# Optimization experiments

Hardware: AMD Instinct MI355X
Metric: run time of the kernel (lower is better)

Reference implementation:

```python
import jax, jax.numpy as jnp
import numpy as np

EPS = 1e-5

def _ternary(w):
    # BitNet 1.58-bit: per-output-channel scale = median(|W|) (scale_op='median'),
    # quantize to {-1,0,1}*scale with straight-through estimator.
    s = jnp.maximum(jnp.median(jnp.abs(w), axis=(1, 2, 3), keepdims=True), EPS)
    q = jnp.clip(jnp.round(w / s), -1.0, 1.0) * s
    return w + jax.lax.stop_gradient(q - w)

def _conv3x3(x, w):
    # NCHW, OIHW, stride 1, pad 1 (spatial-preserving)
    return jax.lax.conv_general_dilated(
        x, _ternary(w), (1, 1), ((1, 1), (1, 1)),
        dimension_numbers=('NCHW', 'OIHW', 'NCHW'))

def _bn(y, g, b, m, v):
    # eval-mode BatchNorm2d folded to a single scale/shift
    inv = g / jnp.sqrt(v + EPS)
    return y * inv[None, :, None, None] + (b - m * inv)[None, :, None, None]

def _ssh(x, p):
    (w3, g3, b3, m3, v3,
     ws, gs, bs, ms, vs,
     w5, g5, b5, m5, v5,
     w7a, g7a, b7a, m7a, v7a,
     w7b, g7b, b7b, m7b, v7b) = p
    c3 = _bn(_conv3x3(x, w3), g3, b3, m3, v3)                      # [B, half, H, W]
    stem = jax.nn.silu(_bn(_conv3x3(x, ws), gs, bs, ms, vs))       # [B, quart, H, W]
    c5 = _bn(_conv3x3(stem, w5), g5, b5, m5, v5)                   # [B, quart, H, W]
    t = jax.nn.silu(_bn(_conv3x3(stem, w7a), g7a, b7a, m7a, v7a))
    c7 = _bn(_conv3x3(t, w7b), g7b, b7b, m7b, v7b)                 # [B, quart, H, W]
    return jax.nn.silu(jnp.concatenate((c3, c5, c7), axis=1))      # [B, out_ch, H, W]

def setup_inputs() -> dict:
    key = jax.random.key(0)
    B, CIN, H, W = 32, 256, 64, 64
    HALF, Q = 128, 64  # out_ch=256 -> half=128, quart=64
    d = {"x": jax.random.normal(jax.random.fold_in(key, 0), (B, CIN, H, W), jnp.float32)}

    def mk(i, o, c):
        k0, k1, k2, k3, k4 = jax.random.split(jax.random.fold_in(key, i), 5)
        return (jax.random.normal(k0, (o, c, 3, 3), jnp.float32) * 0.05,
                1.0 + 0.1 * jax.random.normal(k1, (o,), jnp.float32),   # gamma
                0.1 * jax.random.normal(k2, (o,), jnp.float32),          # beta
                0.1 * jax.random.normal(k3, (o,), jnp.float32),          # running mean
                0.5 + jax.random.uniform(k4, (o,), jnp.float32))         # running var > 0

    for name, (o, c), i in [("3", (HALF, CIN), 1), ("s", (Q, CIN), 2),
                            ("5", (Q, Q), 3), ("7a", (Q, Q), 4), ("7b", (Q, Q), 5)]:
        w, g, b, m, v = mk(i, o, c)
        d["w" + name] = w; d["g" + name] = g; d["b" + name] = b
        d["m" + name] = m; d["v" + name] = v
    return d

def reference(x,
              w3, g3, b3, m3, v3,
              ws, gs, bs, ms, vs,
              w5, g5, b5, m5, v5,
              w7a, g7a, b7a, m7a, v7a,
              w7b, g7b, b7b, m7b, v7b):
    return _ssh(x, (w3, g3, b3, m3, v3, ws, gs, bs, ms, vs,
                    w5, g5, b5, m5, v5, w7a, g7a, b7a, m7a, v7a,
                    w7b, g7b, b7b, m7b, v7b))
```

## Files before the change

kernel.cpp:

```cpp
#include <hip/hip_runtime.h>
#include <stdint.h>

#define EPSF 1e-5f

typedef __bf16 bf16;
typedef __attribute__((ext_vector_type(8))) __bf16 bf16x8;
typedef __attribute__((ext_vector_type(4))) float f32x4;

#define GL16(src, dst) __builtin_amdgcn_global_load_lds( \
    (const __attribute__((address_space(1))) void*)(src), \
    (__attribute__((address_space(3))) void*)(dst), 16, 0, 0)
#define MEMFENCE() asm volatile("" ::: "memory")

template<int N> __device__ __forceinline__ void vwait() {
  static_assert(N == 2 || N == 3 || N == 4 || N == 6, "unsupported vmcnt");
  if constexpr (N == 2) asm volatile("s_waitcnt vmcnt(2)" ::: "memory");
  else if constexpr (N == 3) asm volatile("s_waitcnt vmcnt(3)" ::: "memory");
  else if constexpr (N == 4) asm volatile("s_waitcnt vmcnt(4)" ::: "memory");
  else asm volatile("s_waitcnt vmcnt(6)" ::: "memory");
}

struct QArgs {
  const float* w[5];
  const float* g[5];
  const float* bb[5];
  const float* m[5];
  const float* v[5];
  bf16* wpk[3];
  float* alpha[3];
  float* beta[3];
};

__global__ __launch_bounds__(256)
void prep_k(QArgs qa, const float* __restrict__ x, bf16* __restrict__ xT,
            float* __restrict__ zp) {
  __shared__ int red[2][4];
  __shared__ float tile[64 * 66];
  const int tid = threadIdx.x;
  if (blockIdx.x == 0 && tid < 32) zp[tid] = 0.0f;

  if (blockIdx.x < 384) {
    const int blk = blockIdx.x;
    int layer, o;
    if (blk < 128)      { layer = 0; o = blk; }
    else if (blk < 192) { layer = 1; o = blk - 128; }
    else if (blk < 256) { layer = 2; o = blk - 192; }
    else if (blk < 320) { layer = 3; o = blk - 256; }
    else                { layer = 4; o = blk - 320; }
    const int I_[5]     = {256, 256, 64, 64, 64};
    const int gemm_[5]  = {0, 0, 1, 1, 2};
    const int obase_[5] = {0, 128, 0, 64, 0};
    const int gNMT[3]   = {12, 8, 4};
    const int I = I_[layer];
    const int n = I * 9;
    const float* w = qa.w[layer] + (size_t)o * n;

    unsigned key[9];
#pragma unroll
    for (int j = 0; j < 9; ++j) key[j] = 0xFFFFFFFFu;
    {
      int c2 = 0;
      for (int i = tid; i < n; i += 256) key[c2++] = __float_as_uint(fabsf(w[i]));
    }

    const int wv = tid >> 6;
    unsigned pfx[2] = {0u, 0u};
    const int rank0 = n / 2 - 1, rank1 = n / 2;
    int pp = 0;
    for (int bit = 31; bit >= 0; --bit) {
      const unsigned c0 = pfx[0] | (1u << bit);
      const unsigned c1 = pfx[1] | (1u << bit);
      int loc = 0;
#pragma unroll
      for (int j = 0; j < 9; ++j)
        loc += (key[j] < c0 ? 1 : 0) + (key[j] < c1 ? 0x10000 : 0);
      loc += __shfl_xor(loc, 32); loc += __shfl_xor(loc, 16);
      loc += __shfl_xor(loc, 8);  loc += __shfl_xor(loc, 4);
      loc += __shfl_xor(loc, 2);  loc += __shfl_xor(loc, 1);
      if ((tid & 63) == 0) red[pp][wv] = loc;
      __syncthreads();
      const int tot = red[pp][0] + red[pp][1] + red[pp][2] + red[pp][3];
      if ((tot & 0xFFFF) <= rank0) pfx[0] = c0;
      if ((tot >> 16)    <= rank1) pfx[1] = c1;
      pp ^= 1;
    }
    const float s =
        fmaxf(0.5f * (__uint_as_float(pfx[0]) + __uint_as_float(pfx[1])), EPSF);

    const int g  = gemm_[layer];
    const int ob = obase_[layer];
    const int NMT = gNMT[g];
    if (tid == 0) {
      float inv = qa.g[layer][o] / sqrtf(qa.v[layer][o] + EPSF);
      qa.alpha[g][ob + o] = s * inv;
      qa.beta[g][ob + o]  = qa.bb[layer][o] - qa.m[layer][o] * inv;
    }
    const int og  = ob + o;
    const int mt  = og >> 4;
    const int l16 = og & 15;
    bf16* wp = qa.wpk[g];
    for (int i = tid; i < n; i += 256) {
      float t = rintf(w[i] / s);
      t = fmaxf(-1.f, fminf(1.f, t));
      int c = i / 9, pos = i % 9;
      int k = pos * I + c;
      int ks = k >> 5, kq = (k >> 3) & 3, jj = k & 7;
      wp[((size_t)((ks * NMT + mt) * 64 + kq * 16 + l16)) * 8 + jj] = (bf16)t;
    }
    return;
  }

  const int blk = blockIdx.x - 384;
  const int cg = blk & 3;
  const int h  = (blk >> 2) & 63;
  const int b  = blk >> 8;
  const int w4 = (tid & 15) * 4;
  const int cb = tid >> 4;
#pragma unroll
  for (int p = 0; p < 4; ++p) {
    int c = cb + p * 16;
    const float4 v =
        *(const float4*)&x[(((size_t)(b * 256 + cg * 64 + c)) * 64 + h) * 64 + w4];
    tile[(w4 + 0) * 66 + c] = v.x;
    tile[(w4 + 1) * 66 + c] = v.y;
    tile[(w4 + 2) * 66 + c] = v.z;
    tile[(w4 + 3) * 66 + c] = v.w;
  }
  __syncthreads();
#pragma unroll
  for (int p = 0; p < 2; ++p) {
    int id = tid + p * 256;
    int c8 = id & 7, w2 = id >> 3;
    const float* src = &tile[w2 * 66 + c8 * 8];
    float2 f0 = *(const float2*)(src + 0);
    float2 f1 = *(const float2*)(src + 2);
    float2 f2 = *(const float2*)(src + 4);
    float2 f3 = *(const float2*)(src + 6);
    bf16x8 v;
    v[0] = (bf16)f0.x; v[1] = (bf16)f0.y; v[2] = (bf16)f1.x; v[3] = (bf16)f1.y;
    v[4] = (bf16)f2.x; v[5] = (bf16)f2.y; v[6] = (bf16)f3.x; v[7] = (bf16)f3.y;
    *(bf16x8*)&xT[(((size_t)(b * 64 + h)) * 64 + w2) * 256 + cg * 64 + c8 * 8] = v;
  }
}

template<int CIN, int NMT, int MM, int C1, bool HASPAD, int TPB, int RB, bool XSWZ>
__global__ __launch_bounds__(TPB, 4)
void conv_k(const bf16* __restrict__ xin,
            const bf16* __restrict__ wpk,
            const float* __restrict__ alpha,
            const float* __restrict__ beta,
            float* __restrict__ out, int chan_off,
            bf16* __restrict__ padout,
            const bf16* __restrict__ zpage) {
  constexpr int NC    = CIN / 32;
  constexpr int NPAIR = NC / 2;
  constexpr int NG    = NMT / MM;
  constexpr int RS    = RB + 2;
  constexpr int NCHK  = RS * 66 * 4;
  constexpr int SLOTS = (RB == 2) ? 1088 : 1600;
  constexpr int SUBB  = SLOTS * 16;
  constexpr int BUFB  = 2 * SUBB;
  constexpr int NBUF  = (NPAIR > 1) ? 2 : 1;
  constexpr int P     = (NCHK + TPB - 1) / TPB;
  constexpr int HT    = 64 / RB;
  constexpr int NBLK  = 32 * HT;

  __shared__ __align__(16) union U {
    char xs[NBUF * BUFB];
    bf16 ep[RB * 64 * 72];
  } sm;

  const int tid  = threadIdx.x;
  const int wave = tid >> 6;
  const int lane = tid & 63;
  const int q    = lane >> 4;
  const int t16  = lane & 15;
  const int rw   = wave / NG;
  const int mt0  = (wave % NG) * MM;
  const int wg   = (int)blockIdx.x;
  const int wgid = XSWZ ? (wg & 7) * (NBLK / 8) + (wg >> 3) : wg;
  const int b    = wgid / HT;
  const int h0   = (wgid % HT) * RB;

  const bf16* srcp[P];
  int step[P];
#pragma unroll
  for (int p = 0; p < P; ++p) {
    const int id = tid + p * TPB;
    const int c8p = id & 3, rj = id >> 2;
    const int j = rj % 66, r = rj / 66;
    const int hh = h0 + r - 1, ww = j - 1;
    const bool v = (id < NCHK) && ((unsigned)hh < 64u) && ((unsigned)ww < 64u);
    const int c8 = c8p ^ ((j >> 1) & 3);
    srcp[p] = v ? &xin[(((size_t)(b * 64 + hh)) * 64 + ww) * CIN + c8 * 8] : zpage;
    step[p] = v ? 32 : 0;
  }

  auto stagepair = [&](char* base) {
#pragma unroll
    for (int p = 0; p < P; ++p) {
      if ((p + 1) * TPB <= NCHK || p * TPB + wave * 64 < NCHK) {
        GL16(srcp[p],           base +        (p * TPB + wave * 64) * 16);
        GL16(srcp[p] + step[p], base + SUBB + (p * TPB + wave * 64) * 16);
      }
    }
  };

  int Caddr[3];
#pragma unroll
  for (int kw = 0; kw < 3; ++kw) {
    const int col = t16 + kw;
    Caddr[kw] = rw * 4224 + col * 64 + ((q ^ ((col >> 1) & 3)) << 4);
  }

  char* const lds0 = (char*)&sm.xs[0];

  stagepair(lds0);
  if constexpr (NPAIR > 1) {
#pragma unroll
    for (int p = 0; p < P; ++p) srcp[p] += 2 * step[p];
  }
  MEMFENCE();

  bf16x8 aE[MM], aO[MM];
#pragma unroll
  for (int mm = 0; mm < MM; ++mm)
    aE[mm] = *(const bf16x8*)&wpk[((size_t)(mt0 + mm) * 64 + lane) * 8];

  f32x4 acc[4][MM] = {};
  int tog = BUFB;

  for (int cb = 0; cb < NPAIR; ++cb) {
    if (cb == 0) {
      vwait<MM>();
      __builtin_amdgcn_s_barrier();
    } else {
      vwait<2 * MM>();
      __builtin_amdgcn_s_barrier();
    }
    if constexpr (NPAIR > 1) {
      if (cb + 1 < NPAIR) {
        stagepair(lds0 + (((cb + 1) & 1) ? BUFB : 0));
#pragma unroll
        for (int p = 0; p < P; ++p) srcp[p] += 2 * step[p];
      }
    }
    MEMFENCE();
    __builtin_amdgcn_s_setprio(1);
#pragma unroll
    for (int sub = 0; sub < 2; ++sub) {
      const int ci = 2 * cb + sub;
      bf16x8 bb0[4], bb1[4];
#pragma unroll
      for (int nt = 0; nt < 4; ++nt)
        bb0[nt] = *(const bf16x8*)(lds0 + (Caddr[0] + sub * SUBB + nt * 1024));
#pragma unroll
      for (int pos = 0; pos < 9; ++pos) {
        bf16x8* bc = (pos & 1) ? bb1 : bb0;
        bf16x8* bn = (pos & 1) ? bb0 : bb1;
        if (pos < 8) {
          const int kh1 = (pos + 1) / 3, kw1 = (pos + 1) % 3;
#pragma unroll
          for (int nt = 0; nt < 4; ++nt)
            bn[nt] = *(const bf16x8*)(lds0 +
                (Caddr[kw1] + sub * SUBB + nt * 1024 + kh1 * 4224));
        }
        bf16x8* ac = (pos & 1) ? aO : aE;
        bf16x8* an = (pos & 1) ? aE : aO;
        if (pos < 8) {
          const int ksn = (pos + 1) * NC + ci;
#pragma unroll
          for (int mm = 0; mm < MM; ++mm)
            an[mm] = *(const bf16x8*)&wpk[((size_t)(ksn * NMT + mt0 + mm) * 64 + lane) * 8];
        }
#pragma unroll
        for (int nt = 0; nt < 4; ++nt)
#pragma unroll
          for (int mm = 0; mm < MM; ++mm)
            acc[nt][mm] = __builtin_amdgcn_mfma_f32_16x16x32_bf16(ac[mm], bc[nt], acc[nt][mm], 0, 0, 0);
        if (pos == 8 && ci + 1 < NC) {
#pragma unroll
          for (int mm = 0; mm < MM; ++mm)
            aE[mm] = *(const bf16x8*)&wpk[((size_t)((ci + 1) * NMT + mt0 + mm) * 64 + lane) * 8];
        }
      }
    }
    __builtin_amdgcn_s_setprio(0);
#pragma unroll
    for (int kw = 0; kw < 3; ++kw) Caddr[kw] += tog;
    tog = -tog;
  }

  const int h = h0 + rw;
#pragma unroll
  for (int mm = 0; mm < MM; ++mm) {
    const int o0 = (mt0 + mm) * 16 + 4 * q;
    float av[4], bv2[4];
#pragma unroll
    for (int i = 0; i < 4; ++i) { av[i] = alpha[o0 + i]; bv2[i] = beta[o0 + i]; }
#pragma unroll
    for (int nt = 0; nt < 4; ++nt) {
      const int wv = nt * 16 + t16;
#pragma unroll
      for (int i = 0; i < 4; ++i) {
        float v = acc[nt][mm][i] * av[i] + bv2[i];
        float sg = v / (1.f + __expf(-v));
        acc[nt][mm][i] = sg;
        if (o0 < C1)
          out[(((size_t)(b * 256 + chan_off + o0 + i)) * 64 + h) * 64 + wv] = sg;
      }
    }
  }
  if (HASPAD) {
    __syncthreads();
#pragma unroll
    for (int mm = 0; mm < MM; ++mm) {
      const int o0 = (mt0 + mm) * 16 + 4 * q;
      if (o0 >= C1) {
#pragma unroll
        for (int nt = 0; nt < 4; ++nt) {
          const int px = rw * 64 + nt * 16 + t16;
          union { bf16 h4[4]; uint2 u; } pk;
#pragma unroll
          for (int i = 0; i < 4; ++i) pk.h4[i] = (bf16)acc[nt][mm][i];
          *(uint2*)&sm.ep[px * 72 + (o0 - C1)] = pk.u;
        }
      }
    }
    __syncthreads();
    constexpr int EPP = (RB * 64 * 8) / TPB;
#pragma unroll
    for (int p = 0; p < EPP; ++p) {
      int id = tid + p * TPB;
      int c8 = id & 7, px = id >> 3;
      bf16x8 v = *(const bf16x8*)&sm.ep[px * 72 + c8 * 8];
      const int r = px >> 6, wv2 = px & 63;
      *(bf16x8*)&padout[(((size_t)(b * 64 + h0 + r)) * 64 + wv2) * 64 + c8 * 8] = v;
    }
  }
}

extern "C" void kernel_launch(void* const* d_in, const int* in_sizes, int n_in,
                              void* d_out, int out_size, void* d_ws, size_t ws_size,
                              hipStream_t stream) {
  QArgs qa;
  const float* x = (const float*)d_in[0];
  for (int L = 0; L < 5; ++L) {
    qa.w[L]  = (const float*)d_in[1 + 5 * L];
    qa.g[L]  = (const float*)d_in[2 + 5 * L];
    qa.bb[L] = (const float*)d_in[3 + 5 * L];
    qa.m[L]  = (const float*)d_in[4 + 5 * L];
    qa.v[L]  = (const float*)d_in[5 + 5 * L];
  }
  char* p = (char*)d_ws;
  bf16* wpk1 = (bf16*)p; p += (size_t)192 * 2304 * 2;
  bf16* wpk2 = (bf16*)p; p += (size_t)128 * 576 * 2;
  bf16* wpk3 = (bf16*)p; p += (size_t)64 * 576 * 2;
  float* a1 = (float*)p; p += 1024;
  float* b1 = (float*)p; p += 1024;
  float* a2 = (float*)p; p += 1024;
  float* b2 = (float*)p; p += 1024;
  float* a3 = (float*)p; p += 1024;
  float* b3 = (float*)p; p += 1024;
  float* zp = (float*)p; p += 128;
  bf16* xT   = (bf16*)p; p += (size_t)32 * 64 * 64 * 256 * 2;
  bf16* stem = (bf16*)p; p += (size_t)32 * 64 * 64 * 64 * 2;
  bf16* tbuf = xT;
  qa.wpk[0] = wpk1; qa.wpk[1] = wpk2; qa.wpk[2] = wpk3;
  qa.alpha[0] = a1; qa.alpha[1] = a2; qa.alpha[2] = a3;
  qa.beta[0]  = b1; qa.beta[1]  = b2; qa.beta[2]  = b3;

  prep_k<<<384 + 32 * 64 * 4, 256, 0, stream>>>(qa, x, xT, zp);

  const bf16* zpb = (const bf16*)zp;
  conv_k<256, 12, 3, 128, true,  512, 2, false><<<1024,  512, 0, stream>>>(xT,   wpk1, a1, b1, (float*)d_out, 0,   stem, zpb);
  conv_k< 64,  8, 2,  64, true, 1024, 4, true ><<< 512, 1024, 0, stream>>>(stem, wpk2, a2, b2, (float*)d_out, 128, tbuf, zpb);
  conv_k< 64,  4, 2,  64, false, 512, 4, true ><<< 512,  512, 0, stream>>>(tbuf, wpk3, a3, b3, (float*)d_out, 192, nullptr, zpb);
}
```

Baseline: 422.0 us.

## Add dedicated first-layer conv kernel using 32x32x16 MFMA with repacked weights

Replaces the templated first conv (CIN=256, 192 output channels) with a specialised kernel that uses 32x32x16 bf16 MFMA instead of 16x16x32. The weights are repacked into a matching 32-row tile layout in the prep kernel. Input staging now double-buffers one 32-channel chunk at a time, and weight fragments are prefetched two steps ahead in a three-deep ring. The generic template is simplified to the CIN=64 single-pass path. Larger MFMA tiles should give more reuse per LDS read and fewer instructions, at the cost of more accumulator registers and a more intricate fragment and epilogue index mapping.

```diff
diff --git a/kernel.cpp b/kernel.cpp
--- a/kernel.cpp
+++ b/kernel.cpp
@@ -6,6 +6,7 @@
 typedef __bf16 bf16;
 typedef __attribute__((ext_vector_type(8))) __bf16 bf16x8;
 typedef __attribute__((ext_vector_type(4))) float f32x4;
+typedef __attribute__((ext_vector_type(16))) float f32x16;
 
 #define GL16(src, dst) __builtin_amdgcn_global_load_lds( \
     (const __attribute__((address_space(1))) void*)(src), \
@@ -50,7 +51,7 @@
     const int I_[5]     = {256, 256, 64, 64, 64};
     const int gemm_[5]  = {0, 0, 1, 1, 2};
     const int obase_[5] = {0, 128, 0, 64, 0};
-    const int gNMT[3]   = {12, 8, 4};
+    const int gNMT[3]   = {6, 8, 4};
     const int I = I_[layer];
     const int n = I * 9;
     const float* w = qa.w[layer] + (size_t)o * n;
@@ -96,16 +97,22 @@
       qa.beta[g][ob + o]  = qa.bb[layer][o] - qa.m[layer][o] * inv;
     }
     const int og  = ob + o;
-    const int mt  = og >> 4;
-    const int l16 = og & 15;
     bf16* wp = qa.wpk[g];
     for (int i = tid; i < n; i += 256) {
       float t = rintf(w[i] / s);
       t = fmaxf(-1.f, fminf(1.f, t));
       int c = i / 9, pos = i % 9;
-      int k = pos * I + c;
-      int ks = k >> 5, kq = (k >> 3) & 3, jj = k & 7;
-      wp[((size_t)((ks * NMT + mt) * 64 + kq * 16 + l16)) * 8 + jj] = (bf16)t;
+      if (g == 0) {
+        int ks2 = pos * 16 + (c >> 4);
+        int l   = ((c >> 3) & 1) * 32 + (og & 31);
+        int mt  = og >> 5;
+        wp[((size_t)((ks2 * 6 + mt) * 64 + l)) * 8 + (c & 7)] = (bf16)t;
+      } else {
+        int k = pos * I + c;
+        int ks = k >> 5, kq = (k >> 3) & 3, jj = k & 7;
+        int mt = og >> 4, l16 = og & 15;
+        wp[((size_t)((ks * NMT + mt) * 64 + kq * 16 + l16)) * 8 + jj] = (bf16)t;
+      }
     }
     return;
   }
@@ -143,6 +150,165 @@
   }
 }
 
+__global__ __launch_bounds__(512, 4)
+void conv1_k(const bf16* __restrict__ xin,
+             const bf16* __restrict__ wpk,
+             const float* __restrict__ alpha,
+             const float* __restrict__ beta,
+             float* __restrict__ out,
+             bf16* __restrict__ padout,
+             const bf16* __restrict__ zpage) {
+  __shared__ __align__(16) union U {
+    bf16 xs[2][8704];
+    bf16 ep[128 * 72];
+  } sm;
+
+  const int tid  = threadIdx.x;
+  const int wave = tid >> 6;
+  const int lane = tid & 63;
+  const int l31  = lane & 31;
+  const int b5   = lane >> 5;
+  const int rw   = wave >> 2;
+  const int nn   = (wave >> 1) & 1;
+  const int mg   = wave & 1;
+  const int mt0  = mg * 3;
+  const int b    = blockIdx.x >> 5;
+  const int h0   = (blockIdx.x & 31) << 1;
+
+  const bf16* srcp[3];
+  int step[3];
+#pragma unroll
+  for (int p = 0; p < 3; ++p) {
+    const int id = tid + p * 512;
+    const int c8p = id & 3, rj = id >> 2;
+    const int j = rj % 66, r = rj / 66;
+    const int hh = h0 + r - 1, ww = j - 1;
+    const bool v = (id < 1056) && ((unsigned)hh < 64u) && ((unsigned)ww < 64u);
+    const int c8 = c8p ^ ((j >> 1) & 3);
+    srcp[p] = v ? &xin[(((size_t)(b * 64 + hh)) * 64 + ww) * 256 + c8 * 8] : zpage;
+    step[p] = v ? 32 : 0;
+  }
+  auto stage = [&](char* base) {
+    GL16(srcp[0], base + (tid) * 16);
+    GL16(srcp[1], base + (512 + tid) * 16);
+    if (wave == 0) GL16(srcp[2], base + (1024 + tid) * 16);
+  };
+
+  int Caddr[3];
+#pragma unroll
+  for (int kw = 0; kw < 3; ++kw) {
+    const int col = nn * 32 + l31 + kw;
+    Caddr[kw] = (rw * 66 + col) * 64 + ((b5 ^ ((col >> 1) & 3)) << 4);
+  }
+
+  char* const lds0 = (char*)&sm.xs[0][0];
+
+  stage(lds0);
+  MEMFENCE();
+#pragma unroll
+  for (int p = 0; p < 3; ++p) srcp[p] += step[p];
+
+  const char* wb = (const char*)wpk + lane * 16;
+  bf16x8 fr[3][3];
+#pragma unroll
+  for (int mm = 0; mm < 3; ++mm) {
+    fr[0][mm] = *(const bf16x8*)(wb + (mt0 + mm) * 1024);
+    fr[1][mm] = *(const bf16x8*)(wb + 6144 + (mt0 + mm) * 1024);
+  }
+
+  f32x16 acc[3] = {};
+  int tog = 17408;
+  int cbase = 0;
+
+  for (int ci = 0; ci < 8; ++ci) {
+    vwait<6>();
+    __builtin_amdgcn_s_barrier();
+    if (ci + 1 < 8) {
+      stage(lds0 + (((ci + 1) & 1) ? 17408 : 0));
+#pragma unroll
+      for (int p = 0; p < 3; ++p) srcp[p] += step[p];
+    }
+    MEMFENCE();
+    bf16x8 bb0, bb1;
+    bb0 = *(const bf16x8*)(lds0 + Caddr[0]);
+    __builtin_amdgcn_s_setprio(1);
+#pragma unroll
+    for (int u = 0; u < 18; ++u) {
+      if (u < 17) {
+        const int un = u + 1, posn = un >> 1, kh2n = un & 1;
+        const int khn = posn / 3, kwn = posn % 3;
+        const bf16x8 v =
+            *(const bf16x8*)(lds0 + ((Caddr[kwn] + khn * 4224) ^ (kh2n << 5)));
+        if (un & 1) bb1 = v; else bb0 = v;
+      }
+      const int ut = u + 2;
+      if (ut <= 17) {
+        const int posn = ut >> 1, kh2n = ut & 1;
+#pragma unroll
+        for (int mm = 0; mm < 3; ++mm)
+          fr[ut % 3][mm] = *(const bf16x8*)(wb + cbase + posn * 98304 +
+                                            kh2n * 6144 + (mt0 + mm) * 1024);
+      } else if (ci + 1 < 8) {
+        const int uu = ut - 18, posn = uu >> 1, kh2n = uu & 1;
+#pragma unroll
+        for (int mm = 0; mm < 3; ++mm)
+          fr[ut % 3][mm] = *(const bf16x8*)(wb + cbase + 12288 + posn * 98304 +
+                                            kh2n * 6144 + (mt0 + mm) * 1024);
+      }
+      const bf16x8 bc = (u & 1) ? bb1 : bb0;
+#pragma unroll
+      for (int mm = 0; mm < 3; ++mm)
+        acc[mm] = __builtin_amdgcn_mfma_f32_32x32x16_bf16(fr[u % 3][mm], bc,
+                                                          acc[mm], 0, 0, 0);
+    }
+    __builtin_amdgcn_s_setprio(0);
+#pragma unroll
+    for (int kw = 0; kw < 3; ++kw) Caddr[kw] += tog;
+    tog = -tog;
+    cbase += 12288;
+  }
+
+  const int h  = h0 + rw;
+  const int wv = nn * 32 + l31;
+#pragma unroll
+  for (int mm = 0; mm < 3; ++mm) {
+    const int mt = mt0 + mm, ob = mt * 32;
+#pragma unroll
+    for (int r = 0; r < 16; ++r) {
+      const int o = ob + (r & 3) + 8 * (r >> 2) + 4 * b5;
+      float v = acc[mm][r] * alpha[o] + beta[o];
+      float sg = v / (1.f + __expf(-v));
+      acc[mm][r] = sg;
+      if (ob < 128)
+        out[(((size_t)(b * 256 + o)) * 64 + h) * 64 + wv] = sg;
+    }
+  }
+  __syncthreads();
+  if (mg == 1) {
+    const int px = rw * 64 + nn * 32 + l31;
+#pragma unroll
+    for (int mm = 1; mm < 3; ++mm) {
+      const int mt = mt0 + mm;
+#pragma unroll
+      for (int r4 = 0; r4 < 4; ++r4) {
+        union { bf16 h4[4]; uint2 u; } pk;
+#pragma unroll
+        for (int r2 = 0; r2 < 4; ++r2) pk.h4[r2] = (bf16)acc[mm][r4 * 4 + r2];
+        *(uint2*)&sm.ep[px * 72 + (mt - 4) * 32 + 8 * r4 + 4 * b5] = pk.u;
+      }
+    }
+  }
+  __syncthreads();
+#pragma unroll
+  for (int p = 0; p < 2; ++p) {
+    int id = tid + p * 512;
+    int c8 = id & 7, px = id >> 3;
+    bf16x8 v = *(const bf16x8*)&sm.ep[px * 72 + c8 * 8];
+    const int r = px >> 6, wv2 = px & 63;
+    *(bf16x8*)&padout[(((size_t)(b * 64 + h0 + r)) * 64 + wv2) * 64 + c8 * 8] = v;
+  }
+}
+
 template<int CIN, int NMT, int MM, int C1, bool HASPAD, int TPB, int RB, bool XSWZ>
 __global__ __launch_bounds__(TPB, 4)
 void conv_k(const bf16* __restrict__ xin,
@@ -153,20 +319,18 @@
             bf16* __restrict__ padout,
             const bf16* __restrict__ zpage) {
   constexpr int NC    = CIN / 32;
-  constexpr int NPAIR = NC / 2;
   constexpr int NG    = NMT / MM;
   constexpr int RS    = RB + 2;
   constexpr int NCHK  = RS * 66 * 4;
   constexpr int SLOTS = (RB == 2) ? 1088 : 1600;
   constexpr int SUBB  = SLOTS * 16;
-  constexpr int BUFB  = 2 * SUBB;
-  constexpr int NBUF  = (NPAIR > 1) ? 2 : 1;
   constexpr int P     = (NCHK + TPB - 1) / TPB;
   constexpr int HT    = 64 / RB;
   constexpr int NBLK  = 32 * HT;
+  static_assert(NC == 2, "this template path is for CIN=64 layers");
 
   __shared__ __align__(16) union U {
-    char xs[NBUF * BUFB];
+    char xs[2 * SUBB];
     bf16 ep[RB * 64 * 72];
   } sm;
 
@@ -196,16 +360,6 @@
     step[p] = v ? 32 : 0;
   }
 
-  auto stagepair = [&](char* base) {
-#pragma unroll
-    for (int p = 0; p < P; ++p) {
-      if ((p + 1) * TPB <= NCHK || p * TPB + wave * 64 < NCHK) {
-        GL16(srcp[p],           base +        (p * TPB + wave * 64) * 16);
-        GL16(srcp[p] + step[p], base + SUBB + (p * TPB + wave * 64) * 16);
-      }
-    }
-  };
-
   int Caddr[3];
 #pragma unroll
   for (int kw = 0; kw < 3; ++kw) {
@@ -215,10 +369,12 @@
 
   char* const lds0 = (char*)&sm.xs[0];
 
-  stagepair(lds0);
-  if constexpr (NPAIR > 1) {
-#pragma unroll
-    for (int p = 0; p < P; ++p) srcp[p] += 2 * step[p];
+#pragma unroll
+  for (int p = 0; p < P; ++p) {
+    if ((p + 1) * TPB <= NCHK || p * TPB + wave * 64 < NCHK) {
+      GL16(srcp[p],           lds0 +        (p * TPB + wave * 64) * 16);
+      GL16(srcp[p] + step[p], lds0 + SUBB + (p * TPB + wave * 64) * 16);
+    }
   }
   MEMFENCE();
 
@@ -228,68 +384,49 @@
     aE[mm] = *(const bf16x8*)&wpk[((size_t)(mt0 + mm) * 64 + lane) * 8];
 
   f32x4 acc[4][MM] = {};
-  int tog = BUFB;
-
-  for (int cb = 0; cb < NPAIR; ++cb) {
-    if (cb == 0) {
-      vwait<MM>();
-      __builtin_amdgcn_s_barrier();
-    } else {
-      vwait<2 * MM>();
-      __builtin_amdgcn_s_barrier();
-    }
-    if constexpr (NPAIR > 1) {
-      if (cb + 1 < NPAIR) {
-        stagepair(lds0 + (((cb + 1) & 1) ? BUFB : 0));
-#pragma unroll
-        for (int p = 0; p < P; ++p) srcp[p] += 2 * step[p];
-      }
-    }
-    MEMFENCE();
-    __builtin_amdgcn_s_setprio(1);
-#pragma unroll
-    for (int sub = 0; sub < 2; ++sub) {
-      const int ci = 2 * cb + sub;
-      bf16x8 bb0[4], bb1[4];
+
+  vwait<MM>();
+  __builtin_amdgcn_s_barrier();
+  __builtin_amdgcn_s_setprio(1);
+#pragma unroll
+  for (int sub = 0; sub < 2; ++sub) {
+    const int ci = sub;
+    bf16x8 bb0[4], bb1[4];
+#pragma unroll
+    for (int nt = 0; nt < 4; ++nt)
+      bb0[nt] = *(const bf16x8*)(lds0 + (Caddr[0] + sub * SUBB + nt * 1024));
+#pragma unroll
+    for (int pos = 0; pos < 9; ++pos) {
+      bf16x8* bc = (pos & 1) ? bb1 : bb0;
+      bf16x8* bn = (pos & 1) ? bb0 : bb1;
+      if (pos < 8) {
+        const int kh1 = (pos + 1) / 3, kw1 = (pos + 1) % 3;
+#pragma unroll
+        for (int nt = 0; nt < 4; ++nt)
+          bn[nt] = *(const bf16x8*)(lds0 +
+              (Caddr[kw1] + sub * SUBB + nt * 1024 + kh1 * 4224));
+      }
+      bf16x8* ac = (pos & 1) ? aO : aE;
+      bf16x8* an = (pos & 1) ? aE : aO;
+      if (pos < 8) {
+        const int ksn = (pos + 1) * NC + ci;
+#pragma unroll
+        for (int mm = 0; mm < MM; ++mm)
+          an[mm] = *(const bf16x8*)&wpk[((size_t)(ksn * NMT + mt0 + mm) * 64 + lane) * 8];
+      }
 #pragma unroll
       for (int nt = 0; nt < 4; ++nt)
-        bb0[nt] = *(const bf16x8*)(lds0 + (Caddr[0] + sub * SUBB + nt * 1024));
-#pragma unroll
-      for (int pos = 0; pos < 9; ++pos) {
-        bf16x8* bc = (pos & 1) ? bb1 : bb0;
-        bf16x8* bn = (pos & 1) ? bb0 : bb1;
-        if (pos < 8) {
-          const int kh1 = (pos + 1) / 3, kw1 = (pos + 1) % 3;
-#pragma unroll
-          for (int nt = 0; nt < 4; ++nt)
-            bn[nt] = *(const bf16x8*)(lds0 +
-                (Caddr[kw1] + sub * SUBB + nt * 1024 + kh1 * 4224));
-        }
-        bf16x8* ac = (pos & 1) ? aO : aE;
-        bf16x8* an = (pos & 1) ? aE : aO;
-        if (pos < 8) {
-          const int ksn = (pos + 1) * NC + ci;
-#pragma unroll
-          for (int mm = 0; mm < MM; ++mm)
-            an[mm] = *(const bf16x8*)&wpk[((size_t)(ksn * NMT + mt0 + mm) * 64 + lane) * 8];
-        }
-#pragma unroll
-        for (int nt = 0; nt < 4; ++nt)
-#pragma unroll
-          for (int mm = 0; mm < MM; ++mm)
-            acc[nt][mm] = __builtin_amdgcn_mfma_f32_16x16x32_bf16(ac[mm], bc[nt], acc[nt][mm], 0, 0, 0);
-        if (pos == 8 && ci + 1 < NC) {
-#pragma unroll
-          for (int mm = 0; mm < MM; ++mm)
-            aE[mm] = *(const bf16x8*)&wpk[((size_t)((ci + 1) * NMT + mt0 + mm) * 64 + lane) * 8];
-        }
-      }
-    }
-    __builtin_amdgcn_s_setprio(0);
-#pragma unroll
-    for (int kw = 0; kw < 3; ++kw) Caddr[kw] += tog;
-    tog = -tog;
-  }
+#pragma unroll
+        for (int mm = 0; mm < MM; ++mm)
+          acc[nt][mm] = __builtin_amdgcn_mfma_f32_16x16x32_bf16(ac[mm], bc[nt], acc[nt][mm], 0, 0, 0);
+      if (pos == 8 && ci + 1 < NC) {
+#pragma unroll
+        for (int mm = 0; mm < MM; ++mm)
+          aE[mm] = *(const bf16x8*)&wpk[((size_t)((ci + 1) * NMT + mt0 + mm) * 64 + lane) * 8];
+      }
+    }
+  }
+  __builtin_amdgcn_s_setprio(0);
 
   const int h = h0 + rw;
 #pragma unroll
@@ -373,7 +510,7 @@
   prep_k<<<384 + 32 * 64 * 4, 256, 0, stream>>>(qa, x, xT, zp);
 
   const bf16* zpb = (const bf16*)zp;
-  conv_k<256, 12, 3, 128, true,  512, 2, false><<<1024,  512, 0, stream>>>(xT,   wpk1, a1, b1, (float*)d_out, 0,   stem, zpb);
+  conv1_k<<<1024, 512, 0, stream>>>(xT, wpk1, a1, b1, (float*)d_out, stem, zpb);
   conv_k< 64,  8, 2,  64, true, 1024, 4, true ><<< 512, 1024, 0, stream>>>(stem, wpk2, a2, b2, (float*)d_out, 128, tbuf, zpb);
   conv_k< 64,  4, 2,  64, false, 512, 4, true ><<< 512,  512, 0, stream>>>(tbuf, wpk3, a3, b3, (float*)d_out, 192, nullptr, zpb);
 }
```

Result: slower. 449.4 us (+6.5%).
